# Kernel optimization log

Hardware: AMD Instinct MI355X
Metric: run time of the kernel (lower is better)

The kernel has to match this reference:

```python
import jax, jax.numpy as jnp
import numpy as np

N_NODES = 50000
N_EDGES = 640000
D = 128
L = 3
LN_EPS = 1e-5


def _layer_norm(x, g, b):
    mu = jnp.mean(x, axis=-1, keepdims=True)
    var = jnp.mean(jnp.square(x - mu), axis=-1, keepdims=True)
    return (x - mu) * jax.lax.rsqrt(var + LN_EPS) * g + b


def setup_inputs() -> dict:
    key = jax.random.key(0)
    ks = jax.random.split(key, 8)
    scale = 1.0 / np.sqrt(D)
    x = jax.random.normal(ks[0], (N_NODES, D), dtype=jnp.float32)
    edge_index = jax.random.randint(ks[1], (2, N_EDGES), 0, N_NODES, dtype=jnp.int32)
    return {
        "x": x,
        "edge_index": edge_index,
        "eps": jnp.zeros((L,), jnp.float32),  # GIN epsilon, init 0.0
        "W1": jax.random.normal(ks[2], (L, D, D), jnp.float32) * scale,
        "b1": jnp.zeros((L, D), jnp.float32),
        "W2": jax.random.normal(ks[3], (L, D, D), jnp.float32) * scale,
        "b2": jnp.zeros((L, D), jnp.float32),
        "ln_g": jnp.ones((L, D), jnp.float32),   # per-conv LayerNorm
        "ln_b": jnp.zeros((L, D), jnp.float32),
        "skip_g": jnp.ones((L - 1, D), jnp.float32),  # outer norms for layers 0..L-2
        "skip_b": jnp.zeros((L - 1, D), jnp.float32),
    }


def reference(x, edge_index, eps, W1, b1, W2, b2, ln_g, ln_b, skip_g, skip_b):
    src = edge_index[0]
    dst = edge_index[1]
    h = x  # no input_norm (use_input_norm=False)
    for i in range(L):
        h_in = h
        # scatter-add neighbor aggregation: out[dst] += h[src]
        agg = jax.ops.segment_sum(h[src], dst, num_segments=N_NODES)
        z = (1.0 + eps[i]) * h + agg
        # 2-layer MLP: Linear -> ReLU -> Linear
        z = jnp.maximum(z @ W1[i] + b1[i], 0.0) @ W2[i] + b2[i]
        z = _layer_norm(z, ln_g[i], ln_b[i])
        if i < L - 1:
            z = _layer_norm(z, skip_g[i], skip_b[i])  # skip-path norm
            z = jnp.maximum(z, 0.0)  # ReLU; dropout is identity in eval
        h = z + h_in  # residual (shapes always match: in==hidden)
    return h
```

## Files before the change

kernel.cpp:

```cpp
#include <hip/hip_runtime.h>
#include <hip/hip_bf16.h>

#define N_NODES 50000
#define N_EDGES 640000
#define D 128
#define NPAD 50048
#define LAYERS 3
#define SCAN_NB 196

#define SLAB_HB (N_NODES * 32)
#define SLAB_Z  (NPAD * 32)

typedef __attribute__((ext_vector_type(4))) float f32x4;
typedef __attribute__((ext_vector_type(8))) short bf16x8;
typedef __attribute__((ext_vector_type(4))) short bf16x4;

static __device__ __forceinline__ short f2bf(float f) {
    union { float f; unsigned u; } x; x.f = f;
    unsigned r = x.u + 0x7fffu + ((x.u >> 16) & 1u);
    return (short)(r >> 16);
}
static __device__ __forceinline__ float bf2f(short s) {
    union { unsigned u; float f; } x; x.u = ((unsigned)(unsigned short)s) << 16;
    return x.f;
}

__global__ void init_kernel(const float* __restrict__ x, short* __restrict__ hb) {
    int t = blockIdx.x * 256 + threadIdx.x;
    if (t >= N_NODES * 16) return;
    int node = t >> 4, fg = t & 15;
    int s = fg >> 2, w = (fg & 3) * 8;
    const float* xp = x + (size_t)node * D + fg * 8;
    f32x4 a = *(const f32x4*)(xp);
    f32x4 b = *(const f32x4*)(xp + 4);
    bf16x8 p;
    p[0] = f2bf(a.x); p[1] = f2bf(a.y); p[2] = f2bf(a.z); p[3] = f2bf(a.w);
    p[4] = f2bf(b.x); p[5] = f2bf(b.y); p[6] = f2bf(b.z); p[7] = f2bf(b.w);
    *(bf16x8*)(hb + (size_t)s * SLAB_HB + (size_t)node * 32 + w) = p;
}

__global__ void prepw_kernel(const float* __restrict__ W1, const float* __restrict__ W2,
                             short* __restrict__ wt) {
    int t = blockIdx.x * 256 + threadIdx.x;
    if (t >= 6 * 16384) return;
    int m = t >> 14, rem = t & 16383;
    int c = rem >> 7, k = rem & 127;
    const float* src = (m < 3) ? (W1 + m * 16384) : (W2 + (m - 3) * 16384);
    wt[m * 16384 + c * 128 + k] = f2bf(src[k * 128 + c]);
}

__global__ void hist_kernel(const int* __restrict__ dst, int* __restrict__ deg) {
    int e = blockIdx.x * 256 + threadIdx.x;
    if (e < N_EDGES) atomicAdd(&deg[dst[e]], 1);
}

__global__ void scan1_kernel(const int* __restrict__ deg, int* __restrict__ rs,
                             int* __restrict__ bsum) {
    __shared__ int tmp[256];
    int i = blockIdx.x * 256 + threadIdx.x;
    int v = (i < N_NODES) ? deg[i] : 0;
    tmp[threadIdx.x] = v;
    __syncthreads();
    for (int off = 1; off < 256; off <<= 1) {
        int t = (threadIdx.x >= off) ? tmp[threadIdx.x - off] : 0;
        __syncthreads();
        tmp[threadIdx.x] += t;
        __syncthreads();
    }
    if (i < N_NODES) rs[i] = tmp[threadIdx.x] - v;
    if (threadIdx.x == 255) bsum[blockIdx.x] = tmp[255];
}

__global__ void scan2_kernel(int* __restrict__ bsum) {
    __shared__ int tmp[256];
    int v = (threadIdx.x < SCAN_NB) ? bsum[threadIdx.x] : 0;
    tmp[threadIdx.x] = v;
    __syncthreads();
    for (int off = 1; off < 256; off <<= 1) {
        int t = (threadIdx.x >= off) ? tmp[threadIdx.x - off] : 0;
        __syncthreads();
        tmp[threadIdx.x] += t;
        __syncthreads();
    }
    if (threadIdx.x < SCAN_NB) bsum[threadIdx.x] = tmp[threadIdx.x] - v;
}

__global__ void scan3_kernel(int* __restrict__ rs, const int* __restrict__ bsum) {
    int i = blockIdx.x * 256 + threadIdx.x;
    if (i < N_NODES) rs[i] += bsum[blockIdx.x];
}

__global__ void fill_kernel(const int* __restrict__ src, const int* __restrict__ dst,
                            const int* __restrict__ rs, int* __restrict__ cursor,
                            int* __restrict__ col) {
    int e = blockIdx.x * 256 + threadIdx.x;
    if (e >= N_EDGES) return;
    int d = dst[e];
    int p = atomicAdd(&cursor[d], 1);
    col[rs[d] + p] = src[e];
}

__global__ __launch_bounds__(256) void agg_kernel(const short* __restrict__ hb,
                                                  const int* __restrict__ rs,
                                                  const int* __restrict__ deg,
                                                  const int* __restrict__ col,
                                                  const float* __restrict__ epsArr, int layer,
                                                  short* __restrict__ z) {
    int b = blockIdx.x;
    int j = b & 7, m = b >> 3;
    int slice = j & 3;
    int chunk = 2 * m + (j >> 2);
    int t = threadIdx.x;
    int g = t >> 2, lane4 = t & 3;
    int node = chunk * 64 + g;
    const short* tab = hb + (size_t)slice * SLAB_HB;
    bf16x8 o;
    if (node < N_NODES) {
        float acc[8] = {0.f, 0.f, 0.f, 0.f, 0.f, 0.f, 0.f, 0.f};
        int start = rs[node], dg = deg[node];
        const int* cp = col + start;
        int base = 0;
        for (; base + 8 <= dg; base += 8) {
            bf16x8 v0 = *(const bf16x8*)(tab + (size_t)cp[base + 0] * 32 + lane4 * 8);
            bf16x8 v1 = *(const bf16x8*)(tab + (size_t)cp[base + 1] * 32 + lane4 * 8);
            bf16x8 v2 = *(const bf16x8*)(tab + (size_t)cp[base + 2] * 32 + lane4 * 8);
            bf16x8 v3 = *(const bf16x8*)(tab + (size_t)cp[base + 3] * 32 + lane4 * 8);
            bf16x8 v4 = *(const bf16x8*)(tab + (size_t)cp[base + 4] * 32 + lane4 * 8);
            bf16x8 v5 = *(const bf16x8*)(tab + (size_t)cp[base + 5] * 32 + lane4 * 8);
            bf16x8 v6 = *(const bf16x8*)(tab + (size_t)cp[base + 6] * 32 + lane4 * 8);
            bf16x8 v7 = *(const bf16x8*)(tab + (size_t)cp[base + 7] * 32 + lane4 * 8);
#pragma unroll
            for (int e = 0; e < 8; ++e)
                acc[e] += ((bf2f(v0[e]) + bf2f(v1[e])) + (bf2f(v2[e]) + bf2f(v3[e])))
                        + ((bf2f(v4[e]) + bf2f(v5[e])) + (bf2f(v6[e]) + bf2f(v7[e])));
        }
        for (; base < dg; ++base) {
            bf16x8 v = *(const bf16x8*)(tab + (size_t)cp[base] * 32 + lane4 * 8);
#pragma unroll
            for (int e = 0; e < 8; ++e) acc[e] += bf2f(v[e]);
        }
        float s = 1.0f + epsArr[layer];
        bf16x8 hv = *(const bf16x8*)(tab + (size_t)node * 32 + lane4 * 8);
#pragma unroll
        for (int e = 0; e < 8; ++e) o[e] = f2bf(fmaf(s, bf2f(hv[e]), acc[e]));
    } else {
        o = (bf16x8)(short)0;
    }
    *(bf16x8*)(z + (size_t)slice * SLAB_Z + (size_t)node * 32 + lane4 * 8) = o;
}

template <bool LAST>
__global__ __launch_bounds__(256, 2) void mlp_kernel(const short* __restrict__ Z,
                                                     const short* __restrict__ Wt1,
                                                     const float* __restrict__ B1,
                                                     const short* __restrict__ Wt2,
                                                     const float* __restrict__ B2,
                                                     const float* __restrict__ G1,
                                                     const float* __restrict__ Bt1,
                                                     const float* __restrict__ G2,
                                                     const float* __restrict__ Bt2,
                                                     const float* __restrict__ RS,
                                                     float* __restrict__ H,
                                                     short* __restrict__ HB) {
    __shared__ __align__(16) char lds[49152 + 3072];
    const int t = threadIdx.x;
    const int wave = t >> 6, lane = t & 63;
    const int r = lane & 15, kq = lane >> 4;
    const int lrow = wave * 16 + r;
    const int row = blockIdx.x * 64 + lrow;
    const int swzr = (r & 7) << 4;
    const int swzl = (lrow & 7) << 4;
    const int fcol = kq * 16;

    bf16x8 zb0 = *(const bf16x8*)(Z + (size_t)0 * SLAB_Z + (size_t)row * 32 + kq * 8);
    bf16x8 zb1 = *(const bf16x8*)(Z + (size_t)1 * SLAB_Z + (size_t)row * 32 + kq * 8);
    bf16x8 zb2 = *(const bf16x8*)(Z + (size_t)2 * SLAB_Z + (size_t)row * 32 + kq * 8);
    bf16x8 zb3 = *(const bf16x8*)(Z + (size_t)3 * SLAB_Z + (size_t)row * 32 + kq * 8);
    __builtin_amdgcn_sched_barrier(0);

    bf16x8 g2[8];
    {
        bf16x8 g1[8];
#pragma unroll
        for (int i = 0; i < 8; ++i) g1[i] = *(const bf16x8*)(Wt1 + i * 2048 + t * 8);
#pragma unroll
        for (int i = 0; i < 8; ++i) g2[i] = *(const bf16x8*)(Wt2 + i * 2048 + t * 8);
        if (t < (LAST ? 128 : 192)) {
            int which = t >> 5, chunk = t & 31;
            const float* vp = (which == 0) ? B1 : (which == 1) ? B2 : (which == 2) ? G1
                            : (which == 3) ? Bt1 : (which == 4) ? G2 : Bt2;
            *(f32x4*)(lds + 49152 + which * 512 + chunk * 16) = *(const f32x4*)(vp + chunk * 4);
        }
#pragma unroll
        for (int i = 0; i < 8; ++i) {
            int b = i * 4096 + t * 16;
            *(bf16x8*)(lds + (b ^ (((b >> 8) & 7) << 4))) = g1[i];
        }
    }
    __syncthreads();

    bf16x4 p[8];
#pragma unroll
    for (int ct = 0; ct < 8; ++ct) {
        int wb = (ct * 16 + r) * 256 + kq * 16;
        f32x4 acc = {0.f, 0.f, 0.f, 0.f};
        acc = __builtin_amdgcn_mfma_f32_16x16x32_bf16(*(const bf16x8*)(lds + ((wb      ) ^ swzr)), zb0, acc, 0, 0, 0);
        acc = __builtin_amdgcn_mfma_f32_16x16x32_bf16(*(const bf16x8*)(lds + ((wb +  64) ^ swzr)), zb1, acc, 0, 0, 0);
        acc = __builtin_amdgcn_mfma_f32_16x16x32_bf16(*(const bf16x8*)(lds + ((wb + 128) ^ swzr)), zb2, acc, 0, 0, 0);
        acc = __builtin_amdgcn_mfma_f32_16x16x32_bf16(*(const bf16x8*)(lds + ((wb + 192) ^ swzr)), zb3, acc, 0, 0, 0);
        f32x4 bias = *(const f32x4*)(lds + 49152 + 0 + ct * 64 + fcol);
        p[ct][0] = f2bf(fmaxf(acc[0] + bias.x, 0.0f));
        p[ct][1] = f2bf(fmaxf(acc[1] + bias.y, 0.0f));
        p[ct][2] = f2bf(fmaxf(acc[2] + bias.z, 0.0f));
        p[ct][3] = f2bf(fmaxf(acc[3] + bias.w, 0.0f));
    }
    __syncthreads();

    f32x4 rsv[8] = {};
    if (row < N_NODES) {
#pragma unroll
        for (int ct = 0; ct < 8; ++ct)
            rsv[ct] = *(const f32x4*)(RS + (size_t)row * D + ct * 16 + kq * 4);
    }
    __builtin_amdgcn_sched_barrier(0);

#pragma unroll
    for (int i = 0; i < 8; ++i) {
        int b = i * 4096 + t * 16;
        *(bf16x8*)(lds + (b ^ (((b >> 8) & 7) << 4))) = g2[i];
    }
#pragma unroll
    for (int ct = 0; ct < 8; ++ct)
        *(bf16x4*)(lds + 32768 + ((lrow * 256 + ct * 32 + kq * 8) ^ swzl)) = p[ct];
    __syncthreads();

    bf16x8 hb0 = *(const bf16x8*)(lds + 32768 + ((lrow * 256 +   0 + kq * 16) ^ swzl));
    bf16x8 hb1 = *(const bf16x8*)(lds + 32768 + ((lrow * 256 +  64 + kq * 16) ^ swzl));
    bf16x8 hb2 = *(const bf16x8*)(lds + 32768 + ((lrow * 256 + 128 + kq * 16) ^ swzl));
    bf16x8 hb3 = *(const bf16x8*)(lds + 32768 + ((lrow * 256 + 192 + kq * 16) ^ swzl));

    f32x4 o[8];
#pragma unroll
    for (int ct = 0; ct < 8; ++ct) {
        int wb = (ct * 16 + r) * 256 + kq * 16;
        f32x4 acc = {0.f, 0.f, 0.f, 0.f};
        acc = __builtin_amdgcn_mfma_f32_16x16x32_bf16(*(const bf16x8*)(lds + ((wb      ) ^ swzr)), hb0, acc, 0, 0, 0);
        acc = __builtin_amdgcn_mfma_f32_16x16x32_bf16(*(const bf16x8*)(lds + ((wb +  64) ^ swzr)), hb1, acc, 0, 0, 0);
        acc = __builtin_amdgcn_mfma_f32_16x16x32_bf16(*(const bf16x8*)(lds + ((wb + 128) ^ swzr)), hb2, acc, 0, 0, 0);
        acc = __builtin_amdgcn_mfma_f32_16x16x32_bf16(*(const bf16x8*)(lds + ((wb + 192) ^ swzr)), hb3, acc, 0, 0, 0);
        f32x4 bias = *(const f32x4*)(lds + 49152 + 512 + ct * 64 + fcol);
        o[ct] = acc + bias;
    }

    float s = 0.f, q = 0.f;
#pragma unroll
    for (int ct = 0; ct < 8; ++ct) {
        s += o[ct].x + o[ct].y + o[ct].z + o[ct].w;
        q += o[ct].x * o[ct].x + o[ct].y * o[ct].y + o[ct].z * o[ct].z + o[ct].w * o[ct].w;
    }
    s += __shfl_xor(s, 16, 64); q += __shfl_xor(q, 16, 64);
    s += __shfl_xor(s, 32, 64); q += __shfl_xor(q, 32, 64);
    float mu = s * (1.0f / D);
    float rstd = rsqrtf(q * (1.0f / D) - mu * mu + 1e-5f);
#pragma unroll
    for (int ct = 0; ct < 8; ++ct) {
        f32x4 g = *(const f32x4*)(lds + 49152 + 1024 + ct * 64 + fcol);
        f32x4 b = *(const f32x4*)(lds + 49152 + 1536 + ct * 64 + fcol);
        o[ct] = (o[ct] - mu) * rstd * g + b;
    }

    if (!LAST) {
        float s2 = 0.f, q2 = 0.f;
#pragma unroll
        for (int ct = 0; ct < 8; ++ct) {
            s2 += o[ct].x + o[ct].y + o[ct].z + o[ct].w;
            q2 += o[ct].x * o[ct].x + o[ct].y * o[ct].y + o[ct].z * o[ct].z + o[ct].w * o[ct].w;
        }
        s2 += __shfl_xor(s2, 16, 64); q2 += __shfl_xor(q2, 16, 64);
        s2 += __shfl_xor(s2, 32, 64); q2 += __shfl_xor(q2, 32, 64);
        float mu2 = s2 * (1.0f / D);
        float rstd2 = rsqrtf(q2 * (1.0f / D) - mu2 * mu2 + 1e-5f);
#pragma unroll
        for (int ct = 0; ct < 8; ++ct) {
            f32x4 g = *(const f32x4*)(lds + 49152 + 2048 + ct * 64 + fcol);
            f32x4 b = *(const f32x4*)(lds + 49152 + 2560 + ct * 64 + fcol);
            f32x4 y = (o[ct] - mu2) * rstd2 * g + b;
            y.x = fmaxf(y.x, 0.f); y.y = fmaxf(y.y, 0.f);
            y.z = fmaxf(y.z, 0.f); y.w = fmaxf(y.w, 0.f);
            o[ct] = y;
        }
    }

    if (row < N_NODES) {
#pragma unroll
        for (int ct = 0; ct < 8; ++ct) {
            size_t off = (size_t)row * D + ct * 16 + kq * 4;
            f32x4 hv = rsv[ct] + o[ct];
            *(f32x4*)(H + off) = hv;
            if (!LAST) {
                bf16x4 pb;
                pb[0] = f2bf(hv.x); pb[1] = f2bf(hv.y); pb[2] = f2bf(hv.z); pb[3] = f2bf(hv.w);
                int sl = ct >> 1;
                int w = (ct & 1) * 16 + kq * 4;
                *(bf16x4*)(HB + (size_t)sl * SLAB_HB + (size_t)row * 32 + w) = pb;
            }
        }
    }
}

extern "C" void kernel_launch(void* const* d_in, const int* in_sizes, int n_in,
                              void* d_out, int out_size, void* d_ws, size_t ws_size,
                              hipStream_t stream) {
    const float* x   = (const float*)d_in[0];
    const int*   ei  = (const int*)d_in[1];
    const float* eps = (const float*)d_in[2];
    const float* W1  = (const float*)d_in[3];
    const float* b1  = (const float*)d_in[4];
    const float* W2  = (const float*)d_in[5];
    const float* b2  = (const float*)d_in[6];
    const float* lng = (const float*)d_in[7];
    const float* lnb = (const float*)d_in[8];
    const float* skg = (const float*)d_in[9];
    const float* skb = (const float*)d_in[10];
    float* h = (float*)d_out;

    char* ws = (char*)d_ws;
    short* zbuf = (short*)ws;
    short* hbb  = (short*)(ws + 12812288);
    short* wt   = (short*)(ws + 25612288);
    int*   rs   = (int*)  (ws + 25808896);
    int*   deg  = (int*)  (ws + 26009088);
    int*   cur  = (int*)  (ws + 26209280);
    int*   col  = (int*)  (ws + 26409472);
    int*   bsum = (int*)  (ws + 28969472);

    const int* srcIdx = ei;
    const int* dstIdx = ei + N_EDGES;

    init_kernel<<<(N_NODES * 16 + 255) / 256, 256, 0, stream>>>(x, hbb);
    prepw_kernel<<<(6 * 16384) / 256, 256, 0, stream>>>(W1, W2, wt);

    hipMemsetAsync(deg, 0, 2 * 200192, stream);
    hist_kernel<<<(N_EDGES + 255) / 256, 256, 0, stream>>>(dstIdx, deg);
    scan1_kernel<<<SCAN_NB, 256, 0, stream>>>(deg, rs, bsum);
    scan2_kernel<<<1, 256, 0, stream>>>(bsum);
    scan3_kernel<<<SCAN_NB, 256, 0, stream>>>(rs, bsum);
    fill_kernel<<<(N_EDGES + 255) / 256, 256, 0, stream>>>(srcIdx, dstIdx, rs, cur, col);

    for (int l = 0; l < LAYERS; ++l) {
        agg_kernel<<<391 * 8, 256, 0, stream>>>(
            hbb, rs, deg, col, eps, l, zbuf);
        const float* rsrc = (l == 0) ? x : h;
        if (l < LAYERS - 1) {
            mlp_kernel<false><<<NPAD / 64, 256, 0, stream>>>(
                zbuf, wt + l * 16384, b1 + l * D, wt + (3 + l) * 16384, b2 + l * D,
                lng + l * D, lnb + l * D, skg + l * D, skb + l * D, rsrc, h, hbb);
        } else {
            mlp_kernel<true><<<NPAD / 64, 256, 0, stream>>>(
                zbuf, wt + l * 16384, b1 + l * D, wt + (3 + l) * 16384, b2 + l * D,
                lng + l * D, lnb + l * D, nullptr, nullptr, rsrc, h, nullptr);
        }
    }
}
```

Measured before the change: 226.7 us.

## Split feature table into eight 16-column slabs and use nontemporal loads/stores

Changes the bf16 node-feature layout from four 32-column slabs to eight 16-column slabs. Each slab is then 1.6MB, so the gather working set per aggregation block is smaller and more likely to stay in cache. The aggregation kernel now uses two threads per node and 128 nodes per block, and the MLP kernel's Z loads and HB stores are remapped to the new layout. It also adds nontemporal hints on the column-index reads, the Z writes and reads, and the HB writes. In exchange, each gathered row is only 32 bytes, so the number of separate random accesses doubles.

```diff
diff --git a/kernel.cpp b/kernel.cpp
--- a/kernel.cpp
+++ b/kernel.cpp
@@ -8,8 +8,9 @@
 #define LAYERS 3
 #define SCAN_NB 196
 
-#define SLAB_HB (N_NODES * 32)
-#define SLAB_Z  (NPAD * 32)
+#define NSLAB 8
+#define SLAB_HB (N_NODES * 16)
+#define SLAB_Z  (NPAD * 16)
 
 typedef __attribute__((ext_vector_type(4))) float f32x4;
 typedef __attribute__((ext_vector_type(8))) short bf16x8;
@@ -29,14 +30,14 @@
     int t = blockIdx.x * 256 + threadIdx.x;
     if (t >= N_NODES * 16) return;
     int node = t >> 4, fg = t & 15;
-    int s = fg >> 2, w = (fg & 3) * 8;
+    int s = fg >> 1, w = (fg & 1) * 8;
     const float* xp = x + (size_t)node * D + fg * 8;
     f32x4 a = *(const f32x4*)(xp);
     f32x4 b = *(const f32x4*)(xp + 4);
     bf16x8 p;
     p[0] = f2bf(a.x); p[1] = f2bf(a.y); p[2] = f2bf(a.z); p[3] = f2bf(a.w);
     p[4] = f2bf(b.x); p[5] = f2bf(b.y); p[6] = f2bf(b.z); p[7] = f2bf(b.w);
-    *(bf16x8*)(hb + (size_t)s * SLAB_HB + (size_t)node * 32 + w) = p;
+    *(bf16x8*)(hb + (size_t)s * SLAB_HB + (size_t)node * 16 + w) = p;
 }
 
 __global__ void prepw_kernel(const float* __restrict__ W1, const float* __restrict__ W2,
@@ -107,12 +108,11 @@
                                                   const float* __restrict__ epsArr, int layer,
                                                   short* __restrict__ z) {
     int b = blockIdx.x;
-    int j = b & 7, m = b >> 3;
-    int slice = j & 3;
-    int chunk = 2 * m + (j >> 2);
+    int slice = b & 7;
+    int chunk = b >> 3;
     int t = threadIdx.x;
-    int g = t >> 2, lane4 = t & 3;
-    int node = chunk * 64 + g;
+    int g = t >> 1, lane2 = t & 1;
+    int node = chunk * 128 + g;
     const short* tab = hb + (size_t)slice * SLAB_HB;
     bf16x8 o;
     if (node < N_NODES) {
@@ -121,32 +121,41 @@
         const int* cp = col + start;
         int base = 0;
         for (; base + 8 <= dg; base += 8) {
-            bf16x8 v0 = *(const bf16x8*)(tab + (size_t)cp[base + 0] * 32 + lane4 * 8);
-            bf16x8 v1 = *(const bf16x8*)(tab + (size_t)cp[base + 1] * 32 + lane4 * 8);
-            bf16x8 v2 = *(const bf16x8*)(tab + (size_t)cp[base + 2] * 32 + lane4 * 8);
-            bf16x8 v3 = *(const bf16x8*)(tab + (size_t)cp[base + 3] * 32 + lane4 * 8);
-            bf16x8 v4 = *(const bf16x8*)(tab + (size_t)cp[base + 4] * 32 + lane4 * 8);
-            bf16x8 v5 = *(const bf16x8*)(tab + (size_t)cp[base + 5] * 32 + lane4 * 8);
-            bf16x8 v6 = *(const bf16x8*)(tab + (size_t)cp[base + 6] * 32 + lane4 * 8);
-            bf16x8 v7 = *(const bf16x8*)(tab + (size_t)cp[base + 7] * 32 + lane4 * 8);
+            int c0 = __builtin_nontemporal_load(cp + base + 0);
+            int c1 = __builtin_nontemporal_load(cp + base + 1);
+            int c2 = __builtin_nontemporal_load(cp + base + 2);
+            int c3 = __builtin_nontemporal_load(cp + base + 3);
+            int c4 = __builtin_nontemporal_load(cp + base + 4);
+            int c5 = __builtin_nontemporal_load(cp + base + 5);
+            int c6 = __builtin_nontemporal_load(cp + base + 6);
+            int c7 = __builtin_nontemporal_load(cp + base + 7);
+            bf16x8 v0 = *(const bf16x8*)(tab + (size_t)c0 * 16 + lane2 * 8);
+            bf16x8 v1 = *(const bf16x8*)(tab + (size_t)c1 * 16 + lane2 * 8);
+            bf16x8 v2 = *(const bf16x8*)(tab + (size_t)c2 * 16 + lane2 * 8);
+            bf16x8 v3 = *(const bf16x8*)(tab + (size_t)c3 * 16 + lane2 * 8);
+            bf16x8 v4 = *(const bf16x8*)(tab + (size_t)c4 * 16 + lane2 * 8);
+            bf16x8 v5 = *(const bf16x8*)(tab + (size_t)c5 * 16 + lane2 * 8);
+            bf16x8 v6 = *(const bf16x8*)(tab + (size_t)c6 * 16 + lane2 * 8);
+            bf16x8 v7 = *(const bf16x8*)(tab + (size_t)c7 * 16 + lane2 * 8);
 #pragma unroll
             for (int e = 0; e < 8; ++e)
                 acc[e] += ((bf2f(v0[e]) + bf2f(v1[e])) + (bf2f(v2[e]) + bf2f(v3[e])))
                         + ((bf2f(v4[e]) + bf2f(v5[e])) + (bf2f(v6[e]) + bf2f(v7[e])));
         }
         for (; base < dg; ++base) {
-            bf16x8 v = *(const bf16x8*)(tab + (size_t)cp[base] * 32 + lane4 * 8);
+            int c = __builtin_nontemporal_load(cp + base);
+            bf16x8 v = *(const bf16x8*)(tab + (size_t)c * 16 + lane2 * 8);
 #pragma unroll
             for (int e = 0; e < 8; ++e) acc[e] += bf2f(v[e]);
         }
         float s = 1.0f + epsArr[layer];
-        bf16x8 hv = *(const bf16x8*)(tab + (size_t)node * 32 + lane4 * 8);
+        bf16x8 hv = *(const bf16x8*)(tab + (size_t)node * 16 + lane2 * 8);
 #pragma unroll
         for (int e = 0; e < 8; ++e) o[e] = f2bf(fmaf(s, bf2f(hv[e]), acc[e]));
     } else {
         o = (bf16x8)(short)0;
     }
-    *(bf16x8*)(z + (size_t)slice * SLAB_Z + (size_t)node * 32 + lane4 * 8) = o;
+    __builtin_nontemporal_store(o, (bf16x8*)(z + (size_t)slice * SLAB_Z + (size_t)node * 16 + lane2 * 8));
 }
 
 template <bool LAST>
@@ -171,11 +180,12 @@
     const int swzr = (r & 7) << 4;
     const int swzl = (lrow & 7) << 4;
     const int fcol = kq * 16;
-
-    bf16x8 zb0 = *(const bf16x8*)(Z + (size_t)0 * SLAB_Z + (size_t)row * 32 + kq * 8);
-    bf16x8 zb1 = *(const bf16x8*)(Z + (size_t)1 * SLAB_Z + (size_t)row * 32 + kq * 8);
-    bf16x8 zb2 = *(const bf16x8*)(Z + (size_t)2 * SLAB_Z + (size_t)row * 32 + kq * 8);
-    bf16x8 zb3 = *(const bf16x8*)(Z + (size_t)3 * SLAB_Z + (size_t)row * 32 + kq * 8);
+    const int khalf = kq >> 1, koff = (kq & 1) * 8;
+
+    bf16x8 zb0 = __builtin_nontemporal_load((const bf16x8*)(Z + (size_t)(0 + khalf) * SLAB_Z + (size_t)row * 16 + koff));
+    bf16x8 zb1 = __builtin_nontemporal_load((const bf16x8*)(Z + (size_t)(2 + khalf) * SLAB_Z + (size_t)row * 16 + koff));
+    bf16x8 zb2 = __builtin_nontemporal_load((const bf16x8*)(Z + (size_t)(4 + khalf) * SLAB_Z + (size_t)row * 16 + koff));
+    bf16x8 zb3 = __builtin_nontemporal_load((const bf16x8*)(Z + (size_t)(6 + khalf) * SLAB_Z + (size_t)row * 16 + koff));
     __builtin_amdgcn_sched_barrier(0);
 
     bf16x8 g2[8];
@@ -300,9 +310,8 @@
             if (!LAST) {
                 bf16x4 pb;
                 pb[0] = f2bf(hv.x); pb[1] = f2bf(hv.y); pb[2] = f2bf(hv.z); pb[3] = f2bf(hv.w);
-                int sl = ct >> 1;
-                int w = (ct & 1) * 16 + kq * 4;
-                *(bf16x4*)(HB + (size_t)sl * SLAB_HB + (size_t)row * 32 + w) = pb;
+                __builtin_nontemporal_store(pb,
+                    (bf16x4*)(HB + (size_t)ct * SLAB_HB + (size_t)row * 16 + kq * 4));
             }
         }
     }
```

Result: slower. 304.1 us (+34.2%).
